# Performance work log

Measured on AMD Instinct MI355X. Metric: run time of the kernel, lower is better.

## Reference

```python
import jax, jax.numpy as jnp
import numpy as np

DATA_BITS = 57
SHIFT_BITS = 6
BATCH = 1_000_000


def setup_inputs() -> dict:
    key = jax.random.key(0)
    kx, ks = jax.random.split(key)
    # binary spike bits in {0,1}, stored as float32 (SNN convention)
    X = jax.random.randint(kx, (BATCH, DATA_BITS), 0, 2).astype(jnp.float32)
    shift = jax.random.randint(ks, (BATCH, SHIFT_BITS), 0, 2).astype(jnp.float32)
    return {"X": X, "shift": shift}


def _barrel_shift_right_sticky(X, shift):
    # X: [..., 57] bits, shift: [..., 6] bits (MSB first)
    zeros = jnp.zeros_like(X[..., 0:1])
    current = X
    sticky_accum = zeros
    for layer in range(SHIFT_BITS):
        shift_amt = 2 ** (SHIFT_BITS - 1 - layer)  # 32,16,8,4,2,1 (all <= 57)
        s_bit = shift[..., layer:layer + 1]  # [..., 1]
        # VecORTree over the bits that would be shifted out
        layer_sticky = jnp.max(current[..., DATA_BITS - shift_amt:], axis=-1, keepdims=True)
        # VecMUX(s, layer_sticky, 0) = s * layer_sticky
        layer_sticky_selected = s_bit * layer_sticky
        # VecOR accumulate (binary OR == max for {0,1})
        sticky_accum = jnp.maximum(sticky_accum, layer_sticky_selected)
        # right shift by shift_amt: prepend zeros, drop low bits (shift_amt < 57 always)
        pad = jnp.zeros(current.shape[:-1] + (shift_amt,), dtype=current.dtype)
        shifted = jnp.concatenate([pad, current[..., :-shift_amt]], axis=-1)
        # VecMUX(s, shifted, current)
        current = s_bit * shifted + (1.0 - s_bit) * current
    return current, sticky_accum


def reference(X, shift):
    return _barrel_shift_right_sticky(X, shift)
```

## Files before the change

### kernel.cpp

```cpp
#include <hip/hip_runtime.h>
#include <stdint.h>

#define DATA_BITS 57
#define SHIFT_BITS 6
#define ROWS_PER_BLOCK 256
#define BLOCK 256
#define TILE_VEC (ROWS_PER_BLOCK * DATA_BITS / 4)
#define K_FULL (TILE_VEC / BLOCK)
#define K_REM  (TILE_VEC - K_FULL * BLOCK)
#define STILE_VEC (ROWS_PER_BLOCK * SHIFT_BITS / 4)
#define MASK57 ((1ULL << DATA_BITS) - 1ULL)

typedef float floatx4 __attribute__((ext_vector_type(4)));

__device__ __forceinline__ void deposit(unsigned long long* masks, int p, float4 f) {
    uint32_t v = ((__float_as_uint(f.x) >> 23) & 1u)
               | (((__float_as_uint(f.y) >> 23) & 1u) << 1)
               | (((__float_as_uint(f.z) >> 23) & 1u) << 2)
               | (((__float_as_uint(f.w) >> 23) & 1u) << 3);
    if (v) {
        int row = p / DATA_BITS;
        int col = p - row * DATA_BITS;
        unsigned long long val = (unsigned long long)v << col;
        atomicOr(&masks[row], val & MASK57);
        unsigned long long spill = val >> DATA_BITS;
        if (spill) atomicOr(&masks[row + 1], spill);
    }
}

__device__ __forceinline__ floatx4 expand(const unsigned long long* masks, int p) {
    int row = p / DATA_BITS;
    int col = p - row * DATA_BITS;
    unsigned long long m = masks[row] >> col;
    if (col > DATA_BITS - 4)
        m |= masks[row + 1] << (DATA_BITS - col);
    uint32_t c = (uint32_t)m;
    floatx4 f;
    f.x = __uint_as_float((0u - (c        & 1u)) & 0x3F800000u);
    f.y = __uint_as_float((0u - ((c >> 1) & 1u)) & 0x3F800000u);
    f.z = __uint_as_float((0u - ((c >> 2) & 1u)) & 0x3F800000u);
    f.w = __uint_as_float((0u - ((c >> 3) & 1u)) & 0x3F800000u);
    return f;
}

__global__ __launch_bounds__(BLOCK, 4) void barrel57_kernel(
    const float* __restrict__ X, const float* __restrict__ S,
    float* __restrict__ outCur, float* __restrict__ outSticky,
    int batch)
{
    __shared__ unsigned long long masks[ROWS_PER_BLOCK + 1];
    __shared__ float stile[ROWS_PER_BLOCK * SHIFT_BITS];

    const int t = threadIdx.x;
    const long long blockRow0 = (long long)blockIdx.x * ROWS_PER_BLOCK;
    const long long xBase = blockRow0 * DATA_BITS;
    const long long sBase = blockRow0 * SHIFT_BITS;
    const bool fullBlock = (blockRow0 + ROWS_PER_BLOCK <= (long long)batch);

    masks[t] = 0ULL;
    if (t == 0) masks[ROWS_PER_BLOCK] = 0ULL;

    const float4* Xv = (const float4*)X + (xBase >> 2);
    const float4* Sv = (const float4*)S + (sBase >> 2);

    if (fullBlock) {
        float4 f[K_FULL];
        float4 fr;
        #pragma unroll
        for (int k = 0; k < K_FULL; ++k) f[k] = Xv[t + k * BLOCK];
        if (t < K_REM) fr = Xv[t + K_FULL * BLOCK];
        #pragma unroll
        for (int k = 0; k < 2; ++k) {
            int i = t + k * BLOCK;
            if (i < STILE_VEC) *(float4*)&stile[i * 4] = Sv[i];
        }
        __syncthreads();
        #pragma unroll
        for (int k = 0; k < K_FULL; ++k) deposit(masks, (t + k * BLOCK) * 4, f[k]);
        if (t < K_REM) deposit(masks, (t + K_FULL * BLOCK) * 4, fr);
    } else {
        const long long totalX = (long long)batch * DATA_BITS;
        const long long totalS = (long long)batch * SHIFT_BITS;
        for (int i = t; i < STILE_VEC; i += BLOCK)
            if (sBase + (long long)i * 4 < totalS) *(float4*)&stile[i * 4] = Sv[i];
        __syncthreads();
        for (int i = t; i < TILE_VEC; i += BLOCK)
            if (xBase + (long long)i * 4 < totalX) deposit(masks, i * 4, Xv[i]);
    }
    __syncthreads();

    {
        const long long row = blockRow0 + t;
        if (row < batch) {
            unsigned long long mask = masks[t];
            const float* sr = &stile[t * SHIFT_BITS];
            int s = 0;
            #pragma unroll
            for (int l = 0; l < SHIFT_BITS; ++l)
                s |= (int)((__float_as_uint(sr[l]) >> 23) & 1u) << (SHIFT_BITS - 1 - l);
            unsigned long long outm = (mask << s) & MASK57;
            unsigned long long dropped = (s >= DATA_BITS) ? mask : (mask >> (DATA_BITS - s));
            __builtin_nontemporal_store((dropped != 0ULL) ? 1.0f : 0.0f, &outSticky[row]);
            masks[t] = outm;
        }
    }
    __syncthreads();

    floatx4* Ov = (floatx4*)outCur + (xBase >> 2);
    if (fullBlock) {
        #pragma unroll
        for (int k = 0; k < K_FULL; ++k) {
            int i = t + k * BLOCK;
            __builtin_nontemporal_store(expand(masks, i * 4), &Ov[i]);
        }
        if (t < K_REM) {
            int i = t + K_FULL * BLOCK;
            __builtin_nontemporal_store(expand(masks, i * 4), &Ov[i]);
        }
    } else {
        const long long totalX = (long long)batch * DATA_BITS;
        for (int i = t; i < TILE_VEC; i += BLOCK)
            if (xBase + (long long)i * 4 < totalX)
                __builtin_nontemporal_store(expand(masks, i * 4), &Ov[i]);
    }
}

extern "C" void kernel_launch(void* const* d_in, const int* in_sizes, int n_in,
                              void* d_out, int out_size, void* d_ws, size_t ws_size,
                              hipStream_t stream) {
    const float* X = (const float*)d_in[0];
    const float* S = (const float*)d_in[1];
    const int batch = in_sizes[1] / SHIFT_BITS;
    float* outCur = (float*)d_out;
    float* outSticky = outCur + (long long)batch * DATA_BITS;

    const int grid = (batch + ROWS_PER_BLOCK - 1) / ROWS_PER_BLOCK;
    barrel57_kernel<<<grid, BLOCK, 0, stream>>>(X, S, outCur, outSticky, batch);
}
```

Before: 76.05 us.

## Pack input bits with wave ballots instead of shared-memory atomicOr

Replaces the per-float4 shared-memory atomicOr deposit of bits into per-row masks. Each thread now loads one scalar float per iteration, and a wave ballot packs 64 bits into a contiguous word array. Each row's 57-bit mask is then extracted from two adjacent words. This removes LDS atomic contention and the divide/modulo row mapping, at the cost of scalar 4-byte loads instead of float4 loads and 57 ballot iterations per block.

```diff
diff --git a/kernel.cpp b/kernel.cpp
--- a/kernel.cpp
+++ b/kernel.cpp
@@ -5,28 +5,13 @@
 #define SHIFT_BITS 6
 #define ROWS_PER_BLOCK 256
 #define BLOCK 256
-#define TILE_VEC (ROWS_PER_BLOCK * DATA_BITS / 4)
-#define K_FULL (TILE_VEC / BLOCK)
-#define K_REM  (TILE_VEC - K_FULL * BLOCK)
+#define TILE_FLOATS (ROWS_PER_BLOCK * DATA_BITS)
+#define WORDS (TILE_FLOATS / 64)
+#define NITER (TILE_FLOATS / BLOCK)
 #define STILE_VEC (ROWS_PER_BLOCK * SHIFT_BITS / 4)
 #define MASK57 ((1ULL << DATA_BITS) - 1ULL)
 
 typedef float floatx4 __attribute__((ext_vector_type(4)));
-
-__device__ __forceinline__ void deposit(unsigned long long* masks, int p, float4 f) {
-    uint32_t v = ((__float_as_uint(f.x) >> 23) & 1u)
-               | (((__float_as_uint(f.y) >> 23) & 1u) << 1)
-               | (((__float_as_uint(f.z) >> 23) & 1u) << 2)
-               | (((__float_as_uint(f.w) >> 23) & 1u) << 3);
-    if (v) {
-        int row = p / DATA_BITS;
-        int col = p - row * DATA_BITS;
-        unsigned long long val = (unsigned long long)v << col;
-        atomicOr(&masks[row], val & MASK57);
-        unsigned long long spill = val >> DATA_BITS;
-        if (spill) atomicOr(&masks[row + 1], spill);
-    }
-}
 
 __device__ __forceinline__ floatx4 expand(const unsigned long long* masks, int p) {
     int row = p / DATA_BITS;
@@ -48,80 +33,90 @@
     float* __restrict__ outCur, float* __restrict__ outSticky,
     int batch)
 {
-    __shared__ unsigned long long masks[ROWS_PER_BLOCK + 1];
+    __shared__ unsigned long long words[WORDS + 2];
+    __shared__ unsigned long long maskOut[ROWS_PER_BLOCK + 2];
     __shared__ float stile[ROWS_PER_BLOCK * SHIFT_BITS];
 
-    const int t = threadIdx.x;
+    const int t    = threadIdx.x;
+    const int wave = t >> 6;
+    const int lane = t & 63;
     const long long blockRow0 = (long long)blockIdx.x * ROWS_PER_BLOCK;
     const long long xBase = blockRow0 * DATA_BITS;
     const long long sBase = blockRow0 * SHIFT_BITS;
     const bool fullBlock = (blockRow0 + ROWS_PER_BLOCK <= (long long)batch);
 
-    masks[t] = 0ULL;
-    if (t == 0) masks[ROWS_PER_BLOCK] = 0ULL;
+    if (t < 2) { words[WORDS + t] = 0ULL; maskOut[ROWS_PER_BLOCK + t] = 0ULL; }
 
-    const float4* Xv = (const float4*)X + (xBase >> 2);
     const float4* Sv = (const float4*)S + (sBase >> 2);
 
     if (fullBlock) {
-        float4 f[K_FULL];
-        float4 fr;
-        #pragma unroll
-        for (int k = 0; k < K_FULL; ++k) f[k] = Xv[t + k * BLOCK];
-        if (t < K_REM) fr = Xv[t + K_FULL * BLOCK];
         #pragma unroll
         for (int k = 0; k < 2; ++k) {
             int i = t + k * BLOCK;
             if (i < STILE_VEC) *(float4*)&stile[i * 4] = Sv[i];
         }
-        __syncthreads();
+        const float* Xp = X + xBase;
         #pragma unroll
-        for (int k = 0; k < K_FULL; ++k) deposit(masks, (t + k * BLOCK) * 4, f[k]);
-        if (t < K_REM) deposit(masks, (t + K_FULL * BLOCK) * 4, fr);
+        for (int k = 0; k < NITER; ++k) {
+            float x = Xp[k * BLOCK + t];
+            unsigned long long bal = __ballot(x != 0.0f);
+            if (lane == 0) words[4 * k + wave] = bal;
+        }
     } else {
         const long long totalX = (long long)batch * DATA_BITS;
         const long long totalS = (long long)batch * SHIFT_BITS;
         for (int i = t; i < STILE_VEC; i += BLOCK)
             if (sBase + (long long)i * 4 < totalS) *(float4*)&stile[i * 4] = Sv[i];
-        __syncthreads();
-        for (int i = t; i < TILE_VEC; i += BLOCK)
-            if (xBase + (long long)i * 4 < totalX) deposit(masks, i * 4, Xv[i]);
+        for (int k = 0; k < NITER; ++k) {
+            long long g = xBase + (long long)k * BLOCK + t;
+            float x = (g < totalX) ? X[g] : 0.0f;
+            unsigned long long bal = __ballot(x != 0.0f);
+            if (lane == 0) words[4 * k + wave] = bal;
+        }
     }
     __syncthreads();
 
     {
         const long long row = blockRow0 + t;
+        unsigned long long outm = 0ULL;
         if (row < batch) {
-            unsigned long long mask = masks[t];
+            const int bitpos = t * DATA_BITS;
+            const int w0 = bitpos >> 6;
+            const int off = bitpos & 63;
+            unsigned long long mask = words[w0] >> off;
+            if (off) mask |= words[w0 + 1] << (64 - off);
+            mask &= MASK57;
+
             const float* sr = &stile[t * SHIFT_BITS];
             int s = 0;
             #pragma unroll
             for (int l = 0; l < SHIFT_BITS; ++l)
-                s |= (int)((__float_as_uint(sr[l]) >> 23) & 1u) << (SHIFT_BITS - 1 - l);
-            unsigned long long outm = (mask << s) & MASK57;
+                s |= (int)(sr[l] != 0.0f) << (SHIFT_BITS - 1 - l);
+
+            outm = (mask << s) & MASK57;
             unsigned long long dropped = (s >= DATA_BITS) ? mask : (mask >> (DATA_BITS - s));
             __builtin_nontemporal_store((dropped != 0ULL) ? 1.0f : 0.0f, &outSticky[row]);
-            masks[t] = outm;
         }
+        maskOut[t] = outm;
     }
     __syncthreads();
 
     floatx4* Ov = (floatx4*)outCur + (xBase >> 2);
     if (fullBlock) {
         #pragma unroll
-        for (int k = 0; k < K_FULL; ++k) {
+        for (int k = 0; k < NITER / 4; ++k) {
             int i = t + k * BLOCK;
-            __builtin_nontemporal_store(expand(masks, i * 4), &Ov[i]);
+            __builtin_nontemporal_store(expand(maskOut, i * 4), &Ov[i]);
         }
-        if (t < K_REM) {
-            int i = t + K_FULL * BLOCK;
-            __builtin_nontemporal_store(expand(masks, i * 4), &Ov[i]);
+        if (t < (TILE_FLOATS / 4 - (NITER / 4) * BLOCK)) {
+            int i = t + (NITER / 4) * BLOCK;
+            __builtin_nontemporal_store(expand(maskOut, i * 4), &Ov[i]);
         }
     } else {
         const long long totalX = (long long)batch * DATA_BITS;
-        for (int i = t; i < TILE_VEC; i += BLOCK)
+        for (int i = t; i < TILE_FLOATS / 4; i += BLOCK)
             if (xBase + (long long)i * 4 < totalX)
-                __builtin_nontemporal_store(expand(masks, i * 4), &Ov[i]);
+                __builtin_nontemporal_store(expand(maskOut, i * 4), &Ov[i]);
     }
 }
 
```

Result: slower. 83.92 us (+10.3%).
